# Performance work log

Hardware: AMD Instinct MI355X
Metric: run time of the kernel (lower is better)

The kernel has to match this reference:

```python
import jax, jax.numpy as jnp
import numpy as np

# ---- static config (mirrors YOLOH_Expand cfg) ----
H, W = 200, 200            # feature map size
A = 9                      # num_anchors
C = 80                     # num_classes
M = H * W * A              # total anchors
K = 1000                   # topk NMS candidates
STRIDE = 16
CTR_CLAMP = 32.0
CONF_THRESH = 0.05
NMS_THRESH = 0.6
SCALE_CLAMP = float(np.log(1000.0 / 16))  # DEFAULT_SCALE_CLAMP
ANCHOR_SIZES = np.array([[32,32],[64,64],[128,128],[32,64],[64,32],
                         [64,128],[128,64],[128,256],[256,128]], dtype=np.float32)


def make_anchors():
    # generate_anchors: meshgrid (+0.5)*stride centers, tiled anchor sizes -> (M,4) cxcywh
    ys, xs = np.meshgrid(np.arange(H), np.arange(W), indexing='ij')
    xy = (np.stack([xs, ys], -1).reshape(-1, 2).astype(np.float32) + 0.5) * STRIDE  # (HW,2)
    xy = np.repeat(xy[:, None, :], A, axis=1)                                       # (HW,A,2)
    wh = np.broadcast_to(ANCHOR_SIZES[None], (H * W, A, 2)).astype(np.float32)
    return jnp.asarray(np.concatenate([xy, wh], -1).reshape(-1, 4))


def setup_inputs() -> dict:
    key = jax.random.key(0)
    k1, k2 = jax.random.split(key)
    return {
        'cls_pred': jax.random.normal(k1, (1, M, C), jnp.float32) - 2.0,  # logits, mostly low conf
        'reg_pred': jax.random.normal(k2, (1, M, 4), jnp.float32) * 0.5,
        'anchor_boxes': make_anchors(),
    }


def decode_boxes(anchors, reg):
    # decode_boxes: clamped center offset + clamped log-scale wh -> x1y1x2y2
    ctr_off = jnp.clip(reg[..., :2] * anchors[..., 2:], -CTR_CLAMP, CTR_CLAMP)
    ctr_xy = anchors[..., :2] + ctr_off
    dwdh = jnp.minimum(reg[..., 2:], SCALE_CLAMP)
    wh = anchors[..., 2:] * jnp.exp(dwdh)
    return jnp.concatenate([ctr_xy - 0.5 * wh, ctr_xy + 0.5 * wh], axis=-1)


def pairwise_iou(b):
    # exact math of YOLOH_Expand.nms
    x1, y1, x2, y2 = b[:, 0], b[:, 1], b[:, 2], b[:, 3]
    areas = (x2 - x1) * (y2 - y1)
    xx1 = jnp.maximum(x1[:, None], x1[None, :])
    yy1 = jnp.maximum(y1[:, None], y1[None, :])
    xx2 = jnp.minimum(x2[:, None], x2[None, :])
    yy2 = jnp.minimum(y2[:, None], y2[None, :])
    w = jnp.maximum(1e-28, xx2 - xx1)
    h = jnp.maximum(1e-28, yy2 - yy1)
    inter = w * h
    return inter / (areas[:, None] + areas[None, :] - inter + 1e-14)


def greedy_nms_keep(iou, cls_ids, valid):
    # per-class greedy NMS over score-sorted candidates: box i is suppressed if
    # any kept higher-score box j of the same class has IoU > thresh.
    same = cls_ids[:, None] == cls_ids[None, :]           # (K,K)
    idx = jnp.arange(K)

    def body(keep, i):
        prior = idx < i
        sup = jnp.any(keep & prior & same[i] & (iou[i] > NMS_THRESH))
        keep = keep.at[i].set((~sup) & valid[i])
        return keep, None

    keep0 = jnp.zeros((K,), dtype=bool)
    keep, _ = jax.lax.scan(body, keep0, idx)
    return keep


def reference(cls_pred, reg_pred, anchor_boxes):
    scores = jax.nn.sigmoid(cls_pred[0])                  # (M,C)
    boxes = decode_boxes(anchor_boxes, reg_pred[0])       # (M,4)
    # postprocess: per-anchor best class + confidence threshold
    cls_inds = jnp.argmax(scores, axis=1)                 # (M,)
    sc = jnp.max(scores, axis=1)                          # (M,)
    valid = sc >= CONF_THRESH
    # fixed-size top-k candidate set (invalid ranked last)
    _, top_i = jax.lax.top_k(jnp.where(valid, sc, -1.0), K)
    b = boxes[top_i]                                      # (K,4)
    s = sc[top_i]                                         # (K,)
    c = cls_inds[top_i]                                   # (K,)
    v = valid[top_i]                                      # (K,)
    iou = pairwise_iou(b)                                 # (K,K)
    keep = greedy_nms_keep(iou, c, v)                     # (K,) bool
    return b, s * keep.astype(s.dtype), c.astype(jnp.int32), keep
```

## Files before the change

### kernel.cpp

```cpp
#include <hip/hip_runtime.h>
#include <math.h>

typedef unsigned long long u64;
typedef unsigned int u32;

#define M_ANCH 360000
#define NCLS 80
#define KTOP 1000
#define CAP 8192
#define NBINS 65536
#define RREP 8
#define CONF_THRESH 0.05f
#define NMS_THRESH 0.6f
#define CTR_CLAMP 32.0f
#define SCALE_CLAMP 4.1351665567423560f

#define HIST_OFF   0u
#define HIST_BYTES (RREP * NBINS * 4u)
#define MERGED_OFF (HIST_OFF + HIST_BYTES)
#define BLKSUM_OFF (MERGED_OFF + NBINS * 4u)
#define CNT_OFF    (BLKSUM_OFF + 256u)
#define B_OFF      (CNT_OFF + 4u)
#define VW_OFF     (B_OFF + 4u)
#define ZERO_END   (VW_OFF + 128u)
#define CAND_OFF   ZERO_END
#define SC_OFF     (CAND_OFF + CAP * 8u)
#define CLS_OFF    (SC_OFF + M_ANCH * 4u)
#define SSC_OFF    (CLS_OFF + M_ANCH * 4u)
#define SCLS_OFF   (SSC_OFF + KTOP * 4u)
#define SUP_OFF    ((SCLS_OFF + KTOP * 4u + 15u) & ~15u)

__device__ __forceinline__ u32 fkey(float f) {
    u32 u = __float_as_uint(f);
    return (u & 0x80000000u) ? ~u : (u | 0x80000000u);
}

__global__ __launch_bounds__(256) void k_score(const float* __restrict__ cls_pred,
                                               float* __restrict__ sc_all,
                                               int* __restrict__ cls_all,
                                               u32* __restrict__ hist) {
    __shared__ float lm[64 * 21];
    __shared__ int   lc[64 * 21];
    int t = threadIdx.x;
    const float4* p = (const float4*)cls_pred + (size_t)blockIdx.x * 1280;
    float4 v0 = p[t];
    float4 v1 = p[t + 256];
    float4 v2 = p[t + 512];
    float4 v3 = p[t + 768];
    float4 v4 = p[t + 1024];
#pragma unroll
    for (int k = 0; k < 5; k++) {
        float4 v = (k == 0) ? v0 : (k == 1) ? v1 : (k == 2) ? v2 : (k == 3) ? v3 : v4;
        int f = t + 256 * k;
        int a = f / 20;
        int s = f % 20;
        float mv = v.x; int mc = 0;
        if (v.y > mv) { mv = v.y; mc = 1; }
        if (v.z > mv) { mv = v.z; mc = 2; }
        if (v.w > mv) { mv = v.w; mc = 3; }
        lm[a * 21 + s] = mv;
        lc[a * 21 + s] = s * 4 + mc;
    }
    __syncthreads();
    if (t < 64) {
        float mv = -1e30f; int mc = 0;
#pragma unroll
        for (int s = 0; s < 20; s++) {
            float m = lm[t * 21 + s];
            int c = lc[t * 21 + s];
            if (m > mv) { mv = m; mc = c; }
        }
        int a = blockIdx.x * 64 + t;
        float sc = 1.0f / (1.0f + expf(-mv));
        sc_all[a] = sc;
        cls_all[a] = mc;
        float msk = (sc >= CONF_THRESH) ? sc : -1.0f;
        u32 u = fkey(msk);
        atomicAdd(&hist[((blockIdx.x & (RREP - 1)) << 16) + (u >> 16)], 1u);
    }
}

__global__ __launch_bounds__(1024) void k_hsum(const u32* __restrict__ hist,
                                               u32* __restrict__ merged,
                                               u32* __restrict__ blksum) {
    __shared__ u32 red[1024];
    int t = threadIdx.x;
    int b = blockIdx.x * 1024 + t;
    u32 s = 0;
#pragma unroll
    for (int r = 0; r < RREP; r++) s += hist[r * NBINS + b];
    merged[b] = s;
    red[t] = s;
    __syncthreads();
    for (int off = 512; off > 0; off >>= 1) {
        if (t < off) red[t] += red[t + off];
        __syncthreads();
    }
    if (t == 0) blksum[blockIdx.x] = red[0];
}

__global__ __launch_bounds__(1024) void k_boundary(const u32* __restrict__ merged,
                                                   const u32* __restrict__ blksum,
                                                   u32* __restrict__ outB) {
    __shared__ u32 bs[64];
    __shared__ u32 sj, sA;
    __shared__ u32 csum[1024];
    int t = threadIdx.x;
    if (t < 64) bs[t] = blksum[t];
    __syncthreads();
    if (t == 0) {
        u32 cum = 0; u32 j = 0; u32 Aj = 0;
        for (int b = 63; b >= 0; b--) {
            if (cum + bs[b] >= KTOP) { j = (u32)b; Aj = cum; break; }
            cum += bs[b];
        }
        sj = j; sA = Aj;
    }
    __syncthreads();
    u32 j = sj, Aj = sA;
    u32 h = merged[j * 1024 + t];
    csum[t] = h;
    __syncthreads();
    u32 v = h;
    for (int off = 1; off < 1024; off <<= 1) {
        u32 add = (t + off < 1024) ? csum[t + off] : 0u;
        __syncthreads();
        v += add;
        csum[t] = v;
        __syncthreads();
    }
    u32 above = (t == 1023) ? 0u : csum[t + 1];
    if (Aj + above < KTOP && Aj + above + h >= KTOP) outB[0] = j * 1024 + t;
}

__global__ __launch_bounds__(256) void k_compact(const float* __restrict__ sc_all,
                                                 const u32* __restrict__ pB,
                                                 u32* __restrict__ counter,
                                                 u64* __restrict__ cand) {
    int i = blockIdx.x * 256 + threadIdx.x;
    if (i >= M_ANCH) return;
    u32 B = *pB;
    float s = sc_all[i];
    float m = (s >= CONF_THRESH) ? s : -1.0f;
    u32 u = fkey(m);
    if ((u >> 16) >= B) {
        u32 pos = atomicAdd(counter, 1u);
        if (pos < CAP) cand[pos] = ((u64)u << 32) | (u64)(0xFFFFFFFFu - (u32)i);
    }
}

__global__ __launch_bounds__(1024) void k_select(const u64* __restrict__ cand,
                                                 const u32* __restrict__ counter,
                                                 const float* __restrict__ sc_all,
                                                 const int* __restrict__ cls_all,
                                                 const float* __restrict__ reg_pred,
                                                 const float* __restrict__ anchors,
                                                 float* __restrict__ out,
                                                 float* __restrict__ sel_sc,
                                                 int* __restrict__ sel_cls,
                                                 u64* __restrict__ valid_words) {
    __shared__ u64 keys[CAP];
    int t = threadIdx.x;
    u32 n = *counter;
    if (n > CAP) n = CAP;
    u32 P = 1024;
    while (P < n) P <<= 1;
    for (u32 i = t; i < P; i += 1024) keys[i] = (i < n) ? cand[i] : 0ull;
    for (u32 k = 2; k <= P; k <<= 1) {
        for (u32 j = k >> 1; j > 0; j >>= 1) {
            __syncthreads();
            for (u32 i = t; i < P; i += 1024) {
                u32 ixj = i ^ j;
                if (ixj > i) {
                    u64 a = keys[i], b = keys[ixj];
                    bool desc = ((i & k) == 0);
                    if (desc ? (a < b) : (a > b)) { keys[i] = b; keys[ixj] = a; }
                }
            }
        }
    }
    __syncthreads();
    if (t < KTOP) {
        u64 key = keys[t];
        u32 idx = 0xFFFFFFFFu - (u32)(key & 0xFFFFFFFFull);
        if (idx >= M_ANCH) idx = 0;
        float s = sc_all[idx];
        int cl = cls_all[idx];
        float4 a = ((const float4*)anchors)[idx];
        float4 r = ((const float4*)reg_pred)[idx];
        float ox = fminf(fmaxf(r.x * a.z, -CTR_CLAMP), CTR_CLAMP);
        float oy = fminf(fmaxf(r.y * a.w, -CTR_CLAMP), CTR_CLAMP);
        float cx = a.x + ox, cy = a.y + oy;
        float ww = a.z * expf(fminf(r.z, SCALE_CLAMP));
        float hh = a.w * expf(fminf(r.w, SCALE_CLAMP));
        float4 box;
        box.x = cx - 0.5f * ww;
        box.y = cy - 0.5f * hh;
        box.z = cx + 0.5f * ww;
        box.w = cy + 0.5f * hh;
        ((float4*)out)[t] = box;
        out[5 * KTOP + t] = (float)cl;
        sel_sc[t] = s;
        sel_cls[t] = cl;
        if (s >= CONF_THRESH) atomicOr(&valid_words[t >> 6], 1ull << (t & 63));
    }
}

__global__ __launch_bounds__(256) void k_supmat(const float* __restrict__ out,
                                                const int* __restrict__ sel_cls,
                                                u64* __restrict__ sup) {
    int wid = threadIdx.x >> 6;
    int lane = threadIdx.x & 63;
    int g = blockIdx.x * 4 + wid;
    int i = g >> 4;
    int w = g & 15;
    int j = w * 64 + lane;
    int jc = (j < KTOP) ? j : (KTOP - 1);
    float4 bi = ((const float4*)out)[i];
    float4 bj = ((const float4*)out)[jc];
    int ci = sel_cls[i], cj = sel_cls[jc];
    float ai = (bi.z - bi.x) * (bi.w - bi.y);
    float aj = (bj.z - bj.x) * (bj.w - bj.y);
    float xx1 = fmaxf(bi.x, bj.x), yy1 = fmaxf(bi.y, bj.y);
    float xx2 = fminf(bi.z, bj.z), yy2 = fminf(bi.w, bj.w);
    float iw = fmaxf(1e-28f, xx2 - xx1), ih = fmaxf(1e-28f, yy2 - yy1);
    float inter = iw * ih;
    float iou = inter / (ai + aj - inter + 1e-14f);
    bool pred = (j < i) && (ci == cj) && (iou > NMS_THRESH);
    u64 bal = __ballot((int)pred);
    if (lane == 0) sup[g] = bal;
}

__global__ __launch_bounds__(64) void k_nms(const u64* __restrict__ sup,
                                            const u64* __restrict__ valid_words,
                                            const float* __restrict__ sel_sc,
                                            float* __restrict__ out) {
    __shared__ u64 keepA[16];
    int lane = threadIdx.x;
    if (lane < 16) keepA[lane] = 0ull;
    __syncthreads();

    for (int b = 0; b < 16; b++) {
        int row = b * 64 + lane;
        int rowc = (row < KTOP) ? row : (KTOP - 1);
        const ulonglong2* rp = (const ulonglong2*)(sup + (size_t)rowc * 16);
        ulonglong2 q0 = rp[0], q1 = rp[1], q2 = rp[2], q3 = rp[3];
        ulonglong2 q4 = rp[4], q5 = rp[5], q6 = rp[6], q7 = rp[7];
        u64 d = sup[(size_t)rowc * 16 + b];
        u64 vm = valid_words[b];

        u64 acc = (q0.x & keepA[0])  | (q0.y & keepA[1])
                | (q1.x & keepA[2])  | (q1.y & keepA[3])
                | (q2.x & keepA[4])  | (q2.y & keepA[5])
                | (q3.x & keepA[6])  | (q3.y & keepA[7])
                | (q4.x & keepA[8])  | (q4.y & keepA[9])
                | (q5.x & keepA[10]) | (q5.y & keepA[11])
                | (q6.x & keepA[12]) | (q6.y & keepA[13])
                | (q7.x & keepA[14]) | (q7.y & keepA[15]);
        u64 premask = __ballot(acc != 0ull);
        u64 eligible = vm & ~premask;

        u32 dlo = (u32)d, dhi = (u32)(d >> 32);
        u64 kb = 0ull;
#pragma unroll
        for (int j = 0; j < 64; j++) {
            u32 djl = __builtin_amdgcn_readlane(dlo, j);
            u32 djh = __builtin_amdgcn_readlane(dhi, j);
            u64 dj = ((u64)djh << 32) | (u64)djl;
            bool kj = (((eligible >> j) & 1ull) != 0ull) && ((dj & kb) == 0ull);
            kb |= ((u64)(kj ? 1u : 0u)) << j;
        }
        if (lane == 0) keepA[b] = kb;
        __syncthreads();
    }

    for (int t = lane; t < KTOP; t += 64) {
        int kb = (int)((keepA[t >> 6] >> (t & 63)) & 1ull);
        float s = sel_sc[t];
        out[4 * KTOP + t] = kb ? s : 0.0f;
        out[6 * KTOP + t] = (float)kb;
    }
}

extern "C" void kernel_launch(void* const* d_in, const int* in_sizes, int n_in,
                              void* d_out, int out_size, void* d_ws, size_t ws_size,
                              hipStream_t stream) {
    const float* cls_pred = (const float*)d_in[0];
    const float* reg_pred = (const float*)d_in[1];
    const float* anchors  = (const float*)d_in[2];
    float* out = (float*)d_out;
    char* ws = (char*)d_ws;

    u32* hist     = (u32*)(ws + HIST_OFF);
    u32* merged   = (u32*)(ws + MERGED_OFF);
    u32* blksum   = (u32*)(ws + BLKSUM_OFF);
    u32* counter  = (u32*)(ws + CNT_OFF);
    u32* pB       = (u32*)(ws + B_OFF);
    u64* vwords   = (u64*)(ws + VW_OFF);
    u64* cand     = (u64*)(ws + CAND_OFF);
    float* sc_all = (float*)(ws + SC_OFF);
    int* cls_all  = (int*)(ws + CLS_OFF);
    float* sel_sc = (float*)(ws + SSC_OFF);
    int* sel_cls  = (int*)(ws + SCLS_OFF);
    u64* sup      = (u64*)(ws + SUP_OFF);

    hipMemsetAsync(d_ws, 0, ZERO_END, stream);

    int nbs = M_ANCH / 64;
    int nbc = (M_ANCH + 255) / 256;
    k_score<<<nbs, 256, 0, stream>>>(cls_pred, sc_all, cls_all, hist);
    k_hsum<<<NBINS / 1024, 1024, 0, stream>>>(hist, merged, blksum);
    k_boundary<<<1, 1024, 0, stream>>>(merged, blksum, pB);
    k_compact<<<nbc, 256, 0, stream>>>(sc_all, pB, counter, cand);
    k_select<<<1, 1024, 0, stream>>>(cand, counter, sc_all, cls_all, reg_pred,
                                     anchors, out, sel_sc, sel_cls, vwords);
    k_supmat<<<(KTOP * 16) / 4, 256, 0, stream>>>(out, sel_cls, sup);
    k_nms<<<1, 64, 0, stream>>>(sup, vwords, sel_sc, out);
}
```

Before: 320.3 us.

## Replace single-block bitonic sort with parallel rank selection and simplify histogram

```diff
diff --git a/kernel.cpp b/kernel.cpp
--- a/kernel.cpp
+++ b/kernel.cpp
@@ -9,19 +9,16 @@
 #define KTOP 1000
 #define CAP 8192
 #define NBINS 65536
-#define RREP 8
 #define CONF_THRESH 0.05f
 #define NMS_THRESH 0.6f
 #define CTR_CLAMP 32.0f
 #define SCALE_CLAMP 4.1351665567423560f
 
 #define HIST_OFF   0u
-#define HIST_BYTES (RREP * NBINS * 4u)
-#define MERGED_OFF (HIST_OFF + HIST_BYTES)
-#define BLKSUM_OFF (MERGED_OFF + NBINS * 4u)
-#define CNT_OFF    (BLKSUM_OFF + 256u)
+#define HIST_BYTES (NBINS * 4u)
+#define CNT_OFF    (HIST_OFF + HIST_BYTES)
 #define B_OFF      (CNT_OFF + 4u)
-#define VW_OFF     (B_OFF + 4u)
+#define VW_OFF     (B_OFF + 4u + 8u)
 #define ZERO_END   (VW_OFF + 128u)
 #define CAND_OFF   ZERO_END
 #define SC_OFF     (CAND_OFF + CAP * 8u)
@@ -37,8 +34,7 @@
 
 __global__ __launch_bounds__(256) void k_score(const float* __restrict__ cls_pred,
                                                float* __restrict__ sc_all,
-                                               int* __restrict__ cls_all,
-                                               u32* __restrict__ hist) {
+                                               int* __restrict__ cls_all) {
     __shared__ float lm[64 * 21];
     __shared__ int   lc[64 * 21];
     int t = threadIdx.x;
@@ -74,54 +70,34 @@
         float sc = 1.0f / (1.0f + expf(-mv));
         sc_all[a] = sc;
         cls_all[a] = mc;
-        float msk = (sc >= CONF_THRESH) ? sc : -1.0f;
-        u32 u = fkey(msk);
-        atomicAdd(&hist[((blockIdx.x & (RREP - 1)) << 16) + (u >> 16)], 1u);
-    }
-}
-
-__global__ __launch_bounds__(1024) void k_hsum(const u32* __restrict__ hist,
-                                               u32* __restrict__ merged,
-                                               u32* __restrict__ blksum) {
-    __shared__ u32 red[1024];
-    int t = threadIdx.x;
-    int b = blockIdx.x * 1024 + t;
-    u32 s = 0;
-#pragma unroll
-    for (int r = 0; r < RREP; r++) s += hist[r * NBINS + b];
-    merged[b] = s;
-    red[t] = s;
-    __syncthreads();
-    for (int off = 512; off > 0; off >>= 1) {
-        if (t < off) red[t] += red[t + off];
-        __syncthreads();
-    }
-    if (t == 0) blksum[blockIdx.x] = red[0];
-}
-
-__global__ __launch_bounds__(1024) void k_boundary(const u32* __restrict__ merged,
-                                                   const u32* __restrict__ blksum,
+    }
+}
+
+__global__ __launch_bounds__(256) void k_hist(const float* __restrict__ sc_all,
+                                              u32* __restrict__ hist) {
+    int i = blockIdx.x * 256 + threadIdx.x;
+    if (i >= M_ANCH) return;
+    float s = sc_all[i];
+    float m = (s >= CONF_THRESH) ? s : -1.0f;
+    u32 u = fkey(m);
+    atomicAdd(&hist[u >> 16], 1u);
+}
+
+__global__ __launch_bounds__(1024) void k_boundary(const u32* __restrict__ hist,
                                                    u32* __restrict__ outB) {
-    __shared__ u32 bs[64];
-    __shared__ u32 sj, sA;
     __shared__ u32 csum[1024];
     int t = threadIdx.x;
-    if (t < 64) bs[t] = blksum[t];
+    int base = t * 64;
+    const ulonglong2* hp = (const ulonglong2*)(hist + base);
+    u32 mysum = 0;
+#pragma unroll
+    for (int k = 0; k < 16; k++) {
+        ulonglong2 w = hp[k];
+        mysum += (u32)w.x + (u32)(w.x >> 32) + (u32)w.y + (u32)(w.y >> 32);
+    }
+    csum[t] = mysum;
     __syncthreads();
-    if (t == 0) {
-        u32 cum = 0; u32 j = 0; u32 Aj = 0;
-        for (int b = 63; b >= 0; b--) {
-            if (cum + bs[b] >= KTOP) { j = (u32)b; Aj = cum; break; }
-            cum += bs[b];
-        }
-        sj = j; sA = Aj;
-    }
-    __syncthreads();
-    u32 j = sj, Aj = sA;
-    u32 h = merged[j * 1024 + t];
-    csum[t] = h;
-    __syncthreads();
-    u32 v = h;
+    u32 v = mysum;
     for (int off = 1; off < 1024; off <<= 1) {
         u32 add = (t + off < 1024) ? csum[t + off] : 0u;
         __syncthreads();
@@ -129,8 +105,15 @@
         csum[t] = v;
         __syncthreads();
     }
-    u32 above = (t == 1023) ? 0u : csum[t + 1];
-    if (Aj + above < KTOP && Aj + above + h >= KTOP) outB[0] = j * 1024 + t;
+    u32 A = (t == 1023) ? 0u : csum[t + 1];
+    if (A < KTOP && A + mysum >= KTOP) {
+        u32 c = A;
+        for (int k = 63; k >= 0; k--) {
+            u32 h = hist[base + k];
+            if (c + h >= KTOP) { outB[0] = base + k; break; }
+            c += h;
+        }
+    }
 }
 
 __global__ __launch_bounds__(256) void k_compact(const float* __restrict__ sc_all,
@@ -149,40 +132,31 @@
     }
 }
 
-__global__ __launch_bounds__(1024) void k_select(const u64* __restrict__ cand,
-                                                 const u32* __restrict__ counter,
-                                                 const float* __restrict__ sc_all,
-                                                 const int* __restrict__ cls_all,
-                                                 const float* __restrict__ reg_pred,
-                                                 const float* __restrict__ anchors,
-                                                 float* __restrict__ out,
-                                                 float* __restrict__ sel_sc,
-                                                 int* __restrict__ sel_cls,
-                                                 u64* __restrict__ valid_words) {
-    __shared__ u64 keys[CAP];
-    int t = threadIdx.x;
+__global__ __launch_bounds__(64) void k_rank(const u64* __restrict__ cand,
+                                             const u32* __restrict__ counter,
+                                             const float* __restrict__ sc_all,
+                                             const int* __restrict__ cls_all,
+                                             const float* __restrict__ reg_pred,
+                                             const float* __restrict__ anchors,
+                                             float* __restrict__ out,
+                                             float* __restrict__ sel_sc,
+                                             int* __restrict__ sel_cls,
+                                             u64* __restrict__ valid_words) {
     u32 n = *counter;
     if (n > CAP) n = CAP;
-    u32 P = 1024;
-    while (P < n) P <<= 1;
-    for (u32 i = t; i < P; i += 1024) keys[i] = (i < n) ? cand[i] : 0ull;
-    for (u32 k = 2; k <= P; k <<= 1) {
-        for (u32 j = k >> 1; j > 0; j >>= 1) {
-            __syncthreads();
-            for (u32 i = t; i < P; i += 1024) {
-                u32 ixj = i ^ j;
-                if (ixj > i) {
-                    u64 a = keys[i], b = keys[ixj];
-                    bool desc = ((i & k) == 0);
-                    if (desc ? (a < b) : (a > b)) { keys[i] = b; keys[ixj] = a; }
-                }
-            }
-        }
-    }
-    __syncthreads();
-    if (t < KTOP) {
-        u64 key = keys[t];
-        u32 idx = 0xFFFFFFFFu - (u32)(key & 0xFFFFFFFFull);
+    u32 t = blockIdx.x * 64 + threadIdx.x;
+    if (t >= n) return;
+    u64 mykey = cand[t];
+    u32 rank = 0;
+    const ulonglong2* cp = (const ulonglong2*)cand;
+    u32 n4 = n >> 2;
+    for (u32 g = 0; g < n4; g++) {
+        ulonglong2 a = cp[2 * g], b = cp[2 * g + 1];
+        rank += (a.x > mykey) + (a.y > mykey) + (b.x > mykey) + (b.y > mykey);
+    }
+    for (u32 j = n4 * 4; j < n; j++) rank += (cand[j] > mykey);
+    if (rank < KTOP) {
+        u32 idx = 0xFFFFFFFFu - (u32)(mykey & 0xFFFFFFFFull);
         if (idx >= M_ANCH) idx = 0;
         float s = sc_all[idx];
         int cl = cls_all[idx];
@@ -198,11 +172,11 @@
         box.y = cy - 0.5f * hh;
         box.z = cx + 0.5f * ww;
         box.w = cy + 0.5f * hh;
-        ((float4*)out)[t] = box;
-        out[5 * KTOP + t] = (float)cl;
-        sel_sc[t] = s;
-        sel_cls[t] = cl;
-        if (s >= CONF_THRESH) atomicOr(&valid_words[t >> 6], 1ull << (t & 63));
+        ((float4*)out)[rank] = box;
+        out[5 * KTOP + rank] = (float)cl;
+        sel_sc[rank] = s;
+        sel_cls[rank] = cl;
+        if (s >= CONF_THRESH) atomicOr(&valid_words[rank >> 6], 1ull << (rank & 63));
     }
 }
 
@@ -292,8 +266,6 @@
     char* ws = (char*)d_ws;
 
     u32* hist     = (u32*)(ws + HIST_OFF);
-    u32* merged   = (u32*)(ws + MERGED_OFF);
-    u32* blksum   = (u32*)(ws + BLKSUM_OFF);
     u32* counter  = (u32*)(ws + CNT_OFF);
     u32* pB       = (u32*)(ws + B_OFF);
     u64* vwords   = (u64*)(ws + VW_OFF);
@@ -308,12 +280,12 @@
 
     int nbs = M_ANCH / 64;
     int nbc = (M_ANCH + 255) / 256;
-    k_score<<<nbs, 256, 0, stream>>>(cls_pred, sc_all, cls_all, hist);
-    k_hsum<<<NBINS / 1024, 1024, 0, stream>>>(hist, merged, blksum);
-    k_boundary<<<1, 1024, 0, stream>>>(merged, blksum, pB);
+    k_score<<<nbs, 256, 0, stream>>>(cls_pred, sc_all, cls_all);
+    k_hist<<<nbc, 256, 0, stream>>>(sc_all, hist);
+    k_boundary<<<1, 1024, 0, stream>>>(hist, pB);
     k_compact<<<nbc, 256, 0, stream>>>(sc_all, pB, counter, cand);
-    k_select<<<1, 1024, 0, stream>>>(cand, counter, sc_all, cls_all, reg_pred,
-                                     anchors, out, sel_sc, sel_cls, vwords);
+    k_rank<<<CAP / 64, 64, 0, stream>>>(cand, counter, sc_all, cls_all, reg_pred,
+                                        anchors, out, sel_sc, sel_cls, vwords);
     k_supmat<<<(KTOP * 16) / 4, 256, 0, stream>>>(out, sel_cls, sup);
     k_nms<<<1, 64, 0, stream>>>(sup, vwords, sel_sc, out);
 }
```

Result: slower. 735.8 us (+129.7%).
